# Kernel tuning notes

Hardware: AMD Instinct MI355X
Metric: run time of the kernel (lower is better)

Reference implementation:

```python
import jax, jax.numpy as jnp
import numpy as np

N_NODES = 50000
N_EDGES = 640000
HID = 128
LN_EPS = 1e-5


def setup_inputs() -> dict:
    key = jax.random.key(0)
    ks = jax.random.split(key, 8)
    x = jax.random.normal(ks[0], (N_NODES, HID), dtype=jnp.float32)
    edge_index = jax.random.randint(ks[1], (2, N_EDGES), 0, N_NODES, dtype=jnp.int64)
    edge_attr = jax.random.normal(ks[2], (N_EDGES, HID), dtype=jnp.float32)
    # parameters (Kaiming-ish scaling)
    msg_W1 = jax.random.normal(ks[3], (3 * HID, HID), dtype=jnp.float32) / np.sqrt(3 * HID)
    msg_b1 = jnp.zeros((HID,), dtype=jnp.float32)
    msg_W2 = jax.random.normal(ks[4], (HID, HID), dtype=jnp.float32) / np.sqrt(HID)
    msg_b2 = jnp.zeros((HID,), dtype=jnp.float32)
    upd_W1 = jax.random.normal(ks[5], (2 * HID, HID), dtype=jnp.float32) / np.sqrt(2 * HID)
    upd_b1 = jnp.zeros((HID,), dtype=jnp.float32)
    upd_W2 = jax.random.normal(ks[6], (HID, HID), dtype=jnp.float32) / np.sqrt(HID)
    upd_b2 = jnp.zeros((HID,), dtype=jnp.float32)
    ln_gamma = jnp.ones((HID,), dtype=jnp.float32)
    ln_beta = jnp.zeros((HID,), dtype=jnp.float32)
    return {
        'x': x, 'edge_index': edge_index, 'edge_attr': edge_attr,
        'msg_W1': msg_W1, 'msg_b1': msg_b1, 'msg_W2': msg_W2, 'msg_b2': msg_b2,
        'upd_W1': upd_W1, 'upd_b1': upd_b1, 'upd_W2': upd_W2, 'upd_b2': upd_b2,
        'ln_gamma': ln_gamma, 'ln_beta': ln_beta,
    }


def _layer_norm(h, gamma, beta):
    mu = jnp.mean(h, axis=-1, keepdims=True)
    var = jnp.mean(jnp.square(h - mu), axis=-1, keepdims=True)
    return (h - mu) * jax.lax.rsqrt(var + LN_EPS) * gamma + beta


def reference(x, edge_index, edge_attr,
              msg_W1, msg_b1, msg_W2, msg_b2,
              upd_W1, upd_b1, upd_W2, upd_b2,
              ln_gamma, ln_beta):
    src, dst = edge_index[0], edge_index[1]
    # batched per-edge gather + concat: [E, 3*HID]
    msg_in = jnp.concatenate([x[src], x[dst], edge_attr], axis=-1)
    # message MLP (dropout is identity in eval)
    h = jax.nn.relu(msg_in @ msg_W1 + msg_b1)
    messages = h @ msg_W2 + msg_b2  # [E, HID]
    # scatter-add aggregation by destination node
    aggregated = jax.ops.segment_sum(messages, dst, num_segments=x.shape[0])
    # update MLP
    upd_in = jnp.concatenate([x, aggregated], axis=-1)  # [N, 2*HID]
    u = jax.nn.relu(upd_in @ upd_W1 + upd_b1)
    updated = u @ upd_W2 + upd_b2
    return _layer_norm(x + updated, ln_gamma, ln_beta)
```

## Files before the change

### kernel.cpp

```cpp
#include <hip/hip_runtime.h>

#define HID 128

typedef __attribute__((ext_vector_type(8))) short short8;
typedef __attribute__((ext_vector_type(4))) float f32x4;

__device__ __forceinline__ float bf2f(unsigned short u) {
  union { unsigned int u; float f; } c; c.u = ((unsigned int)u) << 16; return c.f;
}
__device__ __forceinline__ unsigned short f2bf(float f) {
  union { float f; unsigned int u; } c; c.f = f;
  unsigned int u = c.u;
  return (unsigned short)((u + 0x7FFFu + ((u >> 16) & 1u)) >> 16);
}
__device__ __forceinline__ float loads(const void* p, size_t i, bool f32) {
  return f32 ? ((const float*)p)[i] : bf2f(((const unsigned short*)p)[i]);
}
__device__ __forceinline__ short8 load_a8(const void* base, size_t row, int k, bool f32) {
  if (!f32) return *(const short8*)((const unsigned short*)base + row * HID + k);
  const float* fp = (const float*)base + row * HID + k;
  f32x4 f0 = *(const f32x4*)fp;
  f32x4 f1 = *(const f32x4*)(fp + 4);
  short8 t;
  t[0] = (short)f2bf(f0[0]); t[1] = (short)f2bf(f0[1]);
  t[2] = (short)f2bf(f0[2]); t[3] = (short)f2bf(f0[3]);
  t[4] = (short)f2bf(f1[0]); t[5] = (short)f2bf(f1[1]);
  t[6] = (short)f2bf(f1[2]); t[7] = (short)f2bf(f1[3]);
  return t;
}

__global__ void detect_kernel(const void* __restrict__ x,
                              const int* __restrict__ eidx,
                              int* __restrict__ flags) {
  __shared__ int bad, oddnz;
  if (threadIdx.x == 0) { bad = 0; oddnz = 0; }
  __syncthreads();
  const unsigned short* xu = (const unsigned short*)x;
  int mybad = 0;
  for (int i = threadIdx.x; i < 4096; i += 256) {
    int ef = (xu[i] >> 7) & 0xFF;
    if (!(ef == 0 || (ef >= 90 && ef <= 140))) mybad++;
  }
  if (mybad) atomicAdd(&bad, mybad);
  if (threadIdx.x < 128) {
    if (eidx[2 * threadIdx.x + 1] != 0) atomicAdd(&oddnz, 1);
  }
  __syncthreads();
  if (threadIdx.x == 0) {
    flags[0] = (bad > 409) ? 1 : 0;
    flags[1] = (oddnz == 0) ? 1 : 0;
  }
}

__device__ __forceinline__ int get_dst(const int* eidx, bool i64, int E, int e) {
  return i64 ? eidx[2 * (E + e)] : eidx[E + e];
}
__device__ __forceinline__ int get_src(const int* eidx, bool i64, int E, int e) {
  return i64 ? eidx[2 * e] : eidx[e];
}

__global__ void zero_out_kernel(unsigned int* __restrict__ out,
                                const int* __restrict__ flags, long long nelem) {
  bool f32 = flags[0] != 0;
  size_t words = (size_t)nelem * (f32 ? 2 : 1) / 2;
  for (size_t w = blockIdx.x * 256ull + threadIdx.x; w < words; w += (size_t)gridDim.x * 256ull)
    out[w] = 0u;
}

__global__ void repack_all(const void* __restrict__ W1, const void* __restrict__ W2,
                           const void* __restrict__ U1, const void* __restrict__ U2,
                           unsigned short* __restrict__ P1, unsigned short* __restrict__ P2,
                           unsigned short* __restrict__ PU1, unsigned short* __restrict__ PU2,
                           const int* __restrict__ flags) {
  const bool f32 = flags[0] != 0;
  int idx = blockIdx.x * 256 + threadIdx.x;
  const int s1 = 384 * 128, s2 = s1 + 128 * 128, s3 = s2 + 256 * 128, s4 = s3 + 128 * 128;
  if (idx >= s4) return;
  const void* W; unsigned short* P; int off;
  if (idx < s1)      { W = W1; P = P1;  off = idx; }
  else if (idx < s2) { W = W2; P = P2;  off = idx - s1; }
  else if (idx < s3) { W = U1; P = PU1; off = idx - s2; }
  else               { W = U2; P = PU2; off = idx - s3; }
  int j = off & 7, lane = (off >> 3) & 63, ct = (off >> 9) & 7, ks = off >> 12;
  int k = ks * 32 + ((lane >> 4) << 3) + j;
  int n = ct * 16 + (lane & 15);
  P[off] = f2bf(loads(W, (size_t)k * 128 + n, f32));
}

__global__ void hist_kernel(const int* __restrict__ eidx, int* __restrict__ counts,
                            const int* __restrict__ flags, int E, int N) {
  const bool i64 = flags[1] != 0;
  int e = blockIdx.x * 256 + threadIdx.x;
  if (e < E) {
    int d = get_dst(eidx, i64, E, e);
    d = min(max(d, 0), N - 1);
    atomicAdd(&counts[d], 1);
  }
}

__global__ __launch_bounds__(1024) void scanA_kernel(const int* __restrict__ cnt,
                                                     int* __restrict__ curb,
                                                     int* __restrict__ bsum, int N) {
  __shared__ int wsum[16], wsum2[16];
  const int tid = threadIdx.x, lane = tid & 63, wid = tid >> 6;
  int i = blockIdx.x * 1024 + tid;
  int v = (i < N) ? cnt[i] : 0;
  int s = v;
#pragma unroll
  for (int off = 1; off < 64; off <<= 1) {
    int t = __shfl_up(s, off, 64);
    if (lane >= off) s += t;
  }
  if (lane == 63) wsum[wid] = s;
  __syncthreads();
  if (wid == 0 && lane < 16) {
    int w = wsum[lane];
#pragma unroll
    for (int off = 1; off < 16; off <<= 1) {
      int t = __shfl_up(w, off, 16);
      if (lane >= off) w += t;
    }
    wsum2[lane] = w;
    if (lane == 15) bsum[blockIdx.x] = w;
  }
  __syncthreads();
  int pre = (wid > 0) ? wsum2[wid - 1] : 0;
  if (i < N) curb[i] = pre + s - v;
}

__global__ void scanB_kernel(int* __restrict__ bsum, int nb) {
  if (threadIdx.x == 0 && blockIdx.x == 0) {
    int run = 0;
    for (int b = 0; b < nb; b++) { int t = bsum[b]; bsum[b] = run; run += t; }
  }
}

__global__ __launch_bounds__(1024) void scanC_kernel(int* __restrict__ curb,
                                                     const int* __restrict__ bsum, int N) {
  int i = blockIdx.x * 1024 + threadIdx.x;
  if (i < N) curb[i] += bsum[blockIdx.x];
}

__global__ void scatter_rank_kernel(const int* __restrict__ eidx, int* __restrict__ cur,
                                    int* __restrict__ rank, int* __restrict__ sdst,
                                    const int* __restrict__ flags, int E, int N) {
  const bool i64 = flags[1] != 0;
  int e = blockIdx.x * 256 + threadIdx.x;
  if (e < E) {
    int d = get_dst(eidx, i64, E, e);
    d = min(max(d, 0), N - 1);
    int pos = atomicAdd(&cur[d], 1);
    rank[e] = pos;
    sdst[pos] = d;
  }
}

__global__ __launch_bounds__(256) void x1_kernel(
    const void* __restrict__ x, const unsigned short* __restrict__ P1,
    const void* __restrict__ b1, unsigned short* __restrict__ X1,
    const int* __restrict__ flags, int N) {
  __shared__ unsigned short hs[64][264];
  const bool f32 = flags[0] != 0;
  const int tid = threadIdx.x, lane = tid & 63, wid = tid >> 6;
  const int l15 = lane & 15, quad = lane >> 4;
  const int base = blockIdx.x * 64;
  int mn = min(base + wid * 16 + l15, N - 1);

  f32x4 zero = {0.f, 0.f, 0.f, 0.f};
  f32x4 acca[8], accb[8];
#pragma unroll
  for (int ct = 0; ct < 8; ct++) { acca[ct] = zero; accb[ct] = zero; }
#pragma unroll
  for (int ks = 0; ks < 4; ks++) {
    short8 a = load_a8(x, (size_t)mn, ks * 32 + quad * 8, f32);
    const unsigned short* wpa = P1 + ((size_t)(ks * 8) * 64 + lane) * 8;
    const unsigned short* wpb = P1 + ((size_t)((ks + 4) * 8) * 64 + lane) * 8;
#pragma unroll
    for (int ct = 0; ct < 8; ct++) {
      short8 ba = *(const short8*)(wpa + ct * 512);
      short8 bb = *(const short8*)(wpb + ct * 512);
      acca[ct] = __builtin_amdgcn_mfma_f32_16x16x32_bf16(a, ba, acca[ct], 0, 0, 0);
      accb[ct] = __builtin_amdgcn_mfma_f32_16x16x32_bf16(a, bb, accb[ct], 0, 0, 0);
    }
  }
#pragma unroll
  for (int ct = 0; ct < 8; ct++) {
    const int col = ct * 16 + l15;
    const float bv = loads(b1, col, f32);
#pragma unroll
    for (int r = 0; r < 4; r++) {
      hs[wid * 16 + quad * 4 + r][col]       = f2bf(acca[ct][r] + bv);
      hs[wid * 16 + quad * 4 + r][128 + col] = f2bf(accb[ct][r]);
    }
  }
  __syncthreads();
  const int row = tid >> 2, part = tid & 3;
  if (base + row < N) {
    unsigned short* op = X1 + (size_t)(base + row) * 256 + part * 64;
#pragma unroll
    for (int j = 0; j < 8; j++)
      *(short8*)(op + j * 8) = *(const short8*)&hs[row][part * 64 + j * 8];
  }
}

__global__ __launch_bounds__(256) void edgeB_kernel(
    const void* __restrict__ eattr, const int* __restrict__ eidx,
    const int* __restrict__ rank, const unsigned short* __restrict__ X1,
    const unsigned short* __restrict__ P1, const unsigned short* __restrict__ P2,
    unsigned short* __restrict__ msgbuf, const int* __restrict__ flags, int E, int N) {
  __shared__ unsigned short hsb[64][136];
  __shared__ int src_s[64], dst_s[64], rank_s[64];
  const bool f32 = flags[0] != 0;
  const bool i64 = flags[1] != 0;
  const int tid = threadIdx.x, lane = tid & 63, wid = tid >> 6;
  const int l15 = lane & 15, quad = lane >> 4;
  const int base = blockIdx.x * 64;

  if (tid < 64) {
    int e = min(base + tid, E - 1);
    int s = get_src(eidx, i64, E, e);
    int d = get_dst(eidx, i64, E, e);
    src_s[tid] = min(max(s, 0), N - 1);
    dst_s[tid] = min(max(d, 0), N - 1);
    rank_s[tid] = rank[e];
  }

  int me = min(base + wid * 16 + l15, E - 1);
  f32x4 zero = {0.f, 0.f, 0.f, 0.f};
  f32x4 acc[8];
#pragma unroll
  for (int ct = 0; ct < 8; ct++) acc[ct] = zero;
#pragma unroll
  for (int ks = 0; ks < 4; ks++) {
    short8 a = load_a8(eattr, (size_t)me, ks * 32 + quad * 8, f32);
    const unsigned short* wp = P1 + ((size_t)((ks + 8) * 8) * 64 + lane) * 8;
#pragma unroll
    for (int ct = 0; ct < 8; ct++) {
      short8 b = *(const short8*)(wp + ct * 512);
      acc[ct] = __builtin_amdgcn_mfma_f32_16x16x32_bf16(a, b, acc[ct], 0, 0, 0);
    }
  }
#pragma unroll
  for (int ct = 0; ct < 8; ct++) {
    const int col = ct * 16 + l15;
#pragma unroll
    for (int r = 0; r < 4; r++)
      hsb[wid * 16 + quad * 4 + r][col] = f2bf(acc[ct][r]);
  }
  __syncthreads();

#pragma unroll
  for (int it = 0; it < 4; it++) {
    const int r = it * 16 + (tid >> 4);
    const int cg = (tid & 15) * 8;
    short8 h8 = *(const short8*)&hsb[r][cg];
    short8 a8 = *(const short8*)(X1 + (size_t)src_s[r] * 256 + cg);
    short8 b8 = *(const short8*)(X1 + (size_t)dst_s[r] * 256 + 128 + cg);
    short8 o;
#pragma unroll
    for (int j = 0; j < 8; j++) {
      float v = bf2f((unsigned short)h8[j]) + bf2f((unsigned short)a8[j])
              + bf2f((unsigned short)b8[j]);
      o[j] = (short)f2bf(fmaxf(v, 0.f));
    }
    *(short8*)&hsb[r][cg] = o;
  }
  __syncthreads();

  f32x4 acc2[8];
#pragma unroll
  for (int ct = 0; ct < 8; ct++) acc2[ct] = zero;
#pragma unroll
  for (int ks = 0; ks < 4; ks++) {
    short8 a = *(const short8*)&hsb[wid * 16 + l15][ks * 32 + quad * 8];
    const unsigned short* wp = P2 + ((size_t)(ks * 8) * 64 + lane) * 8;
#pragma unroll
    for (int ct = 0; ct < 8; ct++) {
      short8 b = *(const short8*)(wp + ct * 512);
      acc2[ct] = __builtin_amdgcn_mfma_f32_16x16x32_bf16(a, b, acc2[ct], 0, 0, 0);
    }
  }
#pragma unroll
  for (int ct = 0; ct < 8; ct++) {
    const int col = ct * 16 + l15;
#pragma unroll
    for (int r = 0; r < 4; r++)
      hsb[wid * 16 + quad * 4 + r][col] = f2bf(acc2[ct][r]);
  }
  __syncthreads();

  const int row = tid >> 2, part = tid & 3;
  if (base + row < E) {
    unsigned short* mp = msgbuf + (size_t)rank_s[row] * HID + part * 32;
#pragma unroll
    for (int j = 0; j < 4; j++)
      *(short8*)(mp + j * 8) = *(const short8*)&hsb[row][part * 32 + j * 8];
  }
}

__global__ __launch_bounds__(256) void reduce_kernel(
    const unsigned short* __restrict__ msgbuf, const int* __restrict__ sdst,
    const void* __restrict__ b2, float* __restrict__ aggf,
    const int* __restrict__ flags, int E) {
  __shared__ int sd[256];
  const bool f32 = flags[0] != 0;
  const int tid = threadIdx.x;
  const int base = blockIdx.x * 256;
  { int e = base + tid; sd[tid] = (e < E) ? sdst[e] : -1; }
  __syncthreads();
  const int pair = tid & 63;
  const int grp = tid >> 6;
  const int c0 = pair * 2;
  const float b2a = loads(b2, c0, f32);
  const float b2b = loads(b2, c0 + 1, f32);
  float sa = 0.f, sb = 0.f; int cnt = 0, cur = -1;
  for (int r = 0; r < 64; r++) {
    const int lr = grp * 64 + r;
    const int d = sd[lr];
    if (d < 0) break;
    if (d != cur) {
      if (cnt > 0) {
        atomicAdd(&aggf[(size_t)cur * HID + c0],     sa + cnt * b2a);
        atomicAdd(&aggf[(size_t)cur * HID + c0 + 1], sb + cnt * b2b);
      }
      sa = sb = 0.f; cnt = 0; cur = d;
    }
    unsigned int u = *(const unsigned int*)(msgbuf + (size_t)(base + lr) * HID + c0);
    sa += bf2f((unsigned short)(u & 0xFFFF));
    sb += bf2f((unsigned short)(u >> 16));
    cnt++;
  }
  if (cnt > 0) {
    atomicAdd(&aggf[(size_t)cur * HID + c0],     sa + cnt * b2a);
    atomicAdd(&aggf[(size_t)cur * HID + c0 + 1], sb + cnt * b2b);
  }
}

__global__ __launch_bounds__(1024) void scan_kernel(const int* __restrict__ counts,
                                                    int* __restrict__ offs, int N) {
  __shared__ int wsum[16];
  __shared__ int wpre[16];
  __shared__ int carry_s;
  const int tid = threadIdx.x, lane = tid & 63, wid = tid >> 6;
  if (tid == 0) carry_s = 0;
  __syncthreads();
  for (int base = 0; base < N; base += 1024) {
    int i = base + tid;
    int v = (i < N) ? counts[i] : 0;
    int s = v;
#pragma unroll
    for (int off = 1; off < 64; off <<= 1) {
      int t = __shfl_up(s, off, 64);
      if (lane >= off) s += t;
    }
    if (lane == 63) wsum[wid] = s;
    __syncthreads();
    if (tid == 0) {
      int run = carry_s;
#pragma unroll
      for (int w = 0; w < 16; w++) { int t = wsum[w]; wpre[w] = run; run += t; }
      carry_s = run;
    }
    __syncthreads();
    if (i < N) offs[i] = wpre[wid] + s - v;
    __syncthreads();
  }
  if (tid == 0) offs[N] = carry_s;
}

__global__ void scatter_kernel(const int* __restrict__ eidx, int* __restrict__ cur,
                               int* __restrict__ ssrc, int* __restrict__ sdst,
                               int* __restrict__ perm,
                               const int* __restrict__ flags, int E, int N) {
  const bool i64 = flags[1] != 0;
  int e = blockIdx.x * 256 + threadIdx.x;
  if (e < E) {
    int d = get_dst(eidx, i64, E, e);
    int s = get_src(eidx, i64, E, e);
    d = min(max(d, 0), N - 1);
    s = min(max(s, 0), N - 1);
    int pos = atomicAdd(&cur[d], 1);
    ssrc[pos] = s;
    sdst[pos] = d;
    perm[pos] = e;
  }
}

__global__ __launch_bounds__(256) void edge_kernel_sorted(
    const void* __restrict__ x, const void* __restrict__ eattr,
    const int* __restrict__ ssrc, const int* __restrict__ sdst,
    const int* __restrict__ perm,
    const unsigned short* __restrict__ P1, const void* __restrict__ b1,
    const unsigned short* __restrict__ P2, const void* __restrict__ b2,
    float* __restrict__ aggf, const int* __restrict__ flags, int E, int N) {
  __shared__ __align__(16) char smem[64 * 132 * 4];
  __shared__ int sdst_s[64];
  unsigned short (*hs)[136] = (unsigned short (*)[136])smem;
  float (*ms)[132] = (float (*)[132])smem;
  const bool f32 = flags[0] != 0;
  const int tid = threadIdx.x, lane = tid & 63, wid = tid >> 6;
  const int l15 = lane & 15, quad = lane >> 4;
  const int base = blockIdx.x * 64;

  if (tid < 64) sdst_s[tid] = sdst[min(base + tid, E - 1)];

  int me = base + wid * 16 + l15;
  if (me >= E) me = E - 1;
  const int src = ssrc[me];
  const int dsm = sdst[me];
  const int pe  = perm[me];

  f32x4 zero = {0.f, 0.f, 0.f, 0.f};
  f32x4 acc[8];
#pragma unroll
  for (int ct = 0; ct < 8; ct++) acc[ct] = zero;
#pragma unroll
  for (int ks = 0; ks < 12; ks++) {
    const int k0 = ks * 32;
    short8 a;
    if (k0 < 128)      a = load_a8(x,     (size_t)src, k0 + quad * 8, f32);
    else if (k0 < 256) a = load_a8(x,     (size_t)dsm, (k0 - 128) + quad * 8, f32);
    else               a = load_a8(eattr, (size_t)pe,  (k0 - 256) + quad * 8, f32);
    const unsigned short* wp = P1 + ((size_t)(ks * 8) * 64 + lane) * 8;
#pragma unroll
    for (int ct = 0; ct < 8; ct++) {
      short8 b = *(const short8*)(wp + ct * 512);
      acc[ct] = __builtin_amdgcn_mfma_f32_16x16x32_bf16(a, b, acc[ct], 0, 0, 0);
    }
  }
#pragma unroll
  for (int ct = 0; ct < 8; ct++) {
    const int col = ct * 16 + l15;
    const float bv = loads(b1, col, f32);
#pragma unroll
    for (int r = 0; r < 4; r++)
      hs[wid * 16 + quad * 4 + r][col] = f2bf(fmaxf(acc[ct][r] + bv, 0.f));
  }
  f32x4 acc2[8];
#pragma unroll
  for (int ct = 0; ct < 8; ct++) acc2[ct] = zero;
#pragma unroll
  for (int ks = 0; ks < 4; ks++) {
    short8 a = *(const short8*)&hs[wid * 16 + l15][ks * 32 + quad * 8];
    const unsigned short* wp = P2 + ((size_t)(ks * 8) * 64 + lane) * 8;
#pragma unroll
    for (int ct = 0; ct < 8; ct++) {
      short8 b = *(const short8*)(wp + ct * 512);
      acc2[ct] = __builtin_amdgcn_mfma_f32_16x16x32_bf16(a, b, acc2[ct], 0, 0, 0);
    }
  }
  float b2v[8];
#pragma unroll
  for (int ct = 0; ct < 8; ct++) b2v[ct] = loads(b2, ct * 16 + l15, f32);
  __syncthreads();
#pragma unroll
  for (int ct = 0; ct < 8; ct++) {
    const int col = ct * 16 + l15;
#pragma unroll
    for (int r = 0; r < 4; r++) {
      const int e = base + wid * 16 + quad * 4 + r;
      ms[wid * 16 + quad * 4 + r][col] = (e < E) ? (acc2[ct][r] + b2v[ct]) : 0.0f;
    }
  }
  __syncthreads();
  const int col  = tid & 127;
  const int half = tid >> 7;
  const int r0 = half * 32;
  float sum = 0.0f;
  int cur = sdst_s[r0];
#pragma unroll 4
  for (int r = r0; r < r0 + 32; r++) {
    int d = sdst_s[r];
    if (d != cur) {
      atomicAdd(&aggf[(size_t)cur * HID + col], sum);
      sum = 0.0f; cur = d;
    }
    sum += ms[r][col];
  }
  atomicAdd(&aggf[(size_t)cur * HID + col], sum);
}

__global__ __launch_bounds__(256) void edge_kernel_plain(
    const void* __restrict__ x, const int* __restrict__ eidx,
    const void* __restrict__ eattr,
    const unsigned short* __restrict__ P1, const void* __restrict__ b1,
    const unsigned short* __restrict__ P2, const void* __restrict__ b2,
    float* __restrict__ aggf, void* __restrict__ out,
    const int* __restrict__ flags, int E, int N, int small_mode) {
  __shared__ unsigned short hs[64][136];
  const bool f32 = flags[0] != 0;
  const bool i64 = flags[1] != 0;
  const int tid = threadIdx.x, lane = tid & 63, wid = tid >> 6;
  const int l15 = lane & 15, quad = lane >> 4;
  const int base = blockIdx.x * 64;

  int me = base + wid * 16 + l15;
  if (me >= E) me = E - 1;
  int src = get_src(eidx, i64, E, me);
  int dsm = get_dst(eidx, i64, E, me);
  src = min(max(src, 0), N - 1);
  dsm = min(max(dsm, 0), N - 1);

  f32x4 zero = {0.f, 0.f, 0.f, 0.f};
  f32x4 acc[8];
#pragma unroll
  for (int ct = 0; ct < 8; ct++) acc[ct] = zero;
#pragma unroll
  for (int ks = 0; ks < 12; ks++) {
    const int k0 = ks * 32;
    short8 a;
    if (k0 < 128)      a = load_a8(x,     (size_t)src, k0 + quad * 8, f32);
    else if (k0 < 256) a = load_a8(x,     (size_t)dsm, (k0 - 128) + quad * 8, f32);
    else               a = load_a8(eattr, (size_t)me,  (k0 - 256) + quad * 8, f32);
    const unsigned short* wp = P1 + ((size_t)(ks * 8) * 64 + lane) * 8;
#pragma unroll
    for (int ct = 0; ct < 8; ct++) {
      short8 b = *(const short8*)(wp + ct * 512);
      acc[ct] = __builtin_amdgcn_mfma_f32_16x16x32_bf16(a, b, acc[ct], 0, 0, 0);
    }
  }
#pragma unroll
  for (int ct = 0; ct < 8; ct++) {
    const int col = ct * 16 + l15;
    const float bv = loads(b1, col, f32);
#pragma unroll
    for (int r = 0; r < 4; r++)
      hs[wid * 16 + quad * 4 + r][col] = f2bf(fmaxf(acc[ct][r] + bv, 0.f));
  }
  __syncthreads();
  f32x4 acc2[8];
#pragma unroll
  for (int ct = 0; ct < 8; ct++) acc2[ct] = zero;
#pragma unroll
  for (int ks = 0; ks < 4; ks++) {
    short8 a = *(const short8*)&hs[wid * 16 + l15][ks * 32 + quad * 8];
    const unsigned short* wp = P2 + ((size_t)(ks * 8) * 64 + lane) * 8;
#pragma unroll
    for (int ct = 0; ct < 8; ct++) {
      short8 b = *(const short8*)(wp + ct * 512);
      acc2[ct] = __builtin_amdgcn_mfma_f32_16x16x32_bf16(a, b, acc2[ct], 0, 0, 0);
    }
  }
  float b2v[8];
#pragma unroll
  for (int ct = 0; ct < 8; ct++) b2v[ct] = loads(b2, ct * 16 + l15, f32);

  if (!small_mode || f32) {
    float* tgt = (!small_mode) ? aggf : (float*)out;
#pragma unroll
    for (int r = 0; r < 4; r++) {
      const int e = base + wid * 16 + quad * 4 + r;
      if (e < E) {
        int d = get_dst(eidx, i64, E, e);
        d = min(max(d, 0), N - 1);
        float* op = tgt + (size_t)d * HID + l15;
#pragma unroll
        for (int ct = 0; ct < 8; ct++) atomicAdd(op + ct * 16, acc2[ct][r] + b2v[ct]);
      }
    }
  } else {
#pragma unroll
    for (int ct = 0; ct < 8; ct++) {
      const int col = ct * 16 + l15;
#pragma unroll
      for (int r = 0; r < 4; r++)
        hs[wid * 16 + quad * 4 + r][col] = f2bf(acc2[ct][r] + b2v[ct]);
    }
    __syncthreads();
    const int row = tid >> 2;
    const int cg  = (tid & 3) * 32;
    const int e = base + row;
    if (e < E) {
      int d = get_dst(eidx, i64, E, e);
      d = min(max(d, 0), N - 1);
      unsigned int* orow = (unsigned int*)out + ((size_t)d * HID >> 1);
#pragma unroll
      for (int p = 0; p < 16; p++) {
        const int col = cg + p * 2;
        const float lo = bf2f(hs[row][col]);
        const float hi = bf2f(hs[row][col + 1]);
        unsigned int* wp = orow + (col >> 1);
        unsigned int old = *wp, assumed;
        do {
          assumed = old;
          unsigned int nv = (unsigned int)f2bf(bf2f((unsigned short)(assumed & 0xFFFF)) + lo)
                          | ((unsigned int)f2bf(bf2f((unsigned short)(assumed >> 16)) + hi) << 16);
          old = atomicCAS(wp, assumed, nv);
        } while (old != assumed);
      }
    }
  }
}

__global__ __launch_bounds__(256) void node_kernel(
    const void* __restrict__ x, const float* __restrict__ aggf,
    const unsigned short* __restrict__ PU1, const void* __restrict__ ub1,
    const unsigned short* __restrict__ PU2, const void* __restrict__ ub2,
    const void* __restrict__ gamma, const void* __restrict__ beta,
    void* __restrict__ out, const int* __restrict__ flags, int N, int small_mode) {
  __shared__ unsigned short hs[64][136];
  const bool f32 = flags[0] != 0;
  const int tid = threadIdx.x, lane = tid & 63, wid = tid >> 6;
  const int l15 = lane & 15, quad = lane >> 4;
  const int base = blockIdx.x * 64;

  int mn = base + wid * 16 + l15;
  if (mn >= N) mn = N - 1;

  const void* aggp = (!small_mode) ? (const void*)aggf : (const void*)out;
  const bool aggF32 = (!small_mode) ? true : f32;

  f32x4 zero = {0.f, 0.f, 0.f, 0.f};
  f32x4 acc[8];
#pragma unroll
  for (int ct = 0; ct < 8; ct++) acc[ct] = zero;
#pragma unroll
  for (int ks = 0; ks < 8; ks++) {
    const int k0 = ks * 32;
    short8 a;
    if (k0 < 128) a = load_a8(x,    (size_t)mn, k0 + quad * 8, f32);
    else          a = load_a8(aggp, (size_t)mn, (k0 - 128) + quad * 8, aggF32);
    const unsigned short* wp = PU1 + ((size_t)(ks * 8) * 64 + lane) * 8;
#pragma unroll
    for (int ct = 0; ct < 8; ct++) {
      short8 b = *(const short8*)(wp + ct * 512);
      acc[ct] = __builtin_amdgcn_mfma_f32_16x16x32_bf16(a, b, acc[ct], 0, 0, 0);
    }
  }
#pragma unroll
  for (int ct = 0; ct < 8; ct++) {
    const int col = ct * 16 + l15;
    const float bv = loads(ub1, col, f32);
#pragma unroll
    for (int r = 0; r < 4; r++)
      hs[wid * 16 + quad * 4 + r][col] = f2bf(fmaxf(acc[ct][r] + bv, 0.f));
  }
  __syncthreads();
  f32x4 acc2[8];
#pragma unroll
  for (int ct = 0; ct < 8; ct++) acc2[ct] = zero;
#pragma unroll
  for (int ks = 0; ks < 4; ks++) {
    short8 a = *(const short8*)&hs[wid * 16 + l15][ks * 32 + quad * 8];
    const unsigned short* wp = PU2 + ((size_t)(ks * 8) * 64 + lane) * 8;
#pragma unroll
    for (int ct = 0; ct < 8; ct++) {
      short8 b = *(const short8*)(wp + ct * 512);
      acc2[ct] = __builtin_amdgcn_mfma_f32_16x16x32_bf16(a, b, acc2[ct], 0, 0, 0);
    }
  }

  float vals[8][4];
  float s1[4] = {0.f, 0.f, 0.f, 0.f};
  float s2[4] = {0.f, 0.f, 0.f, 0.f};
#pragma unroll
  for (int ct = 0; ct < 8; ct++) {
    const int col = ct * 16 + l15;
    const float bv = loads(ub2, col, f32);
#pragma unroll
    for (int r = 0; r < 4; r++) {
      int row = base + wid * 16 + quad * 4 + r;
      int rc = row < N ? row : 0;
      float v = acc2[ct][r] + bv + loads(x, (size_t)rc * HID + col, f32);
      vals[ct][r] = v;
      s1[r] += v;
      s2[r] += v * v;
    }
  }
#pragma unroll
  for (int off = 1; off < 16; off <<= 1) {
#pragma unroll
    for (int r = 0; r < 4; r++) {
      s1[r] += __shfl_xor(s1[r], off, 16);
      s2[r] += __shfl_xor(s2[r], off, 16);
    }
  }
#pragma unroll
  for (int r = 0; r < 4; r++) {
    const int row = base + wid * 16 + quad * 4 + r;
    if (row < N) {
      const float mean = s1[r] * (1.0f / 128.0f);
      const float var  = fmaxf(s2[r] * (1.0f / 128.0f) - mean * mean, 0.0f);
      const float rstd = rsqrtf(var + 1e-5f);
#pragma unroll
      for (int ct = 0; ct < 8; ct++) {
        const int col = ct * 16 + l15;
        float o = (vals[ct][r] - mean) * rstd * loads(gamma, col, f32) + loads(beta, col, f32);
        if (f32) ((float*)out)[(size_t)row * HID + col] = o;
        else     ((unsigned short*)out)[(size_t)row * HID + col] = f2bf(o);
      }
    }
  }
}

extern "C" void kernel_launch(void* const* d_in, const int* in_sizes, int n_in,
                              void* d_out, int out_size, void* d_ws, size_t ws_size,
                              hipStream_t stream) {
  (void)n_in;
  const void* x     = d_in[0];
  const int*  eidx  = (const int*)d_in[1];
  const void* eattr = d_in[2];
  const void* W1  = d_in[3];
  const void* b1  = d_in[4];
  const void* W2  = d_in[5];
  const void* b2  = d_in[6];
  const void* U1  = d_in[7];
  const void* ub1 = d_in[8];
  const void* U2  = d_in[9];
  const void* ub2 = d_in[10];
  const void* gam = d_in[11];
  const void* bet = d_in[12];

  const int N = in_sizes[0] / HID;
  const int E = in_sizes[2] / HID;

  char* ws = (char*)d_ws;
  auto alignup = [](size_t v) { return (v + 255) & ~(size_t)255; };

  int* flags = (int*)ws;
  unsigned short* P1  = (unsigned short*)(ws + 256);
  unsigned short* P2  = (unsigned short*)(ws + 256 + 98304);
  unsigned short* PU1 = (unsigned short*)(ws + 256 + 131072);
  unsigned short* PU2 = (unsigned short*)(ws + 256 + 196608);
  const size_t agg_off = 256 + 229376;
  float* aggf = (float*)(ws + agg_off);
  const size_t agg_bytes = (size_t)N * HID * sizeof(float);
  const size_t need_basic = agg_off + agg_bytes;

  size_t o3 = alignup(need_basic);
  size_t cnt_off  = o3; o3 = alignup(o3 + (size_t)(N + 64) * 4);
  size_t cur_off  = o3; o3 = alignup(o3 + (size_t)(N + 64) * 4);
  size_t bsum_off = o3; o3 = alignup(o3 + 1024);
  size_t rank_off = o3; o3 = alignup(o3 + (size_t)E * 4);
  size_t sds3_off = o3; o3 = alignup(o3 + (size_t)E * 4);
  size_t x1_off   = o3; o3 = alignup(o3 + (size_t)N * 256 * 2);
  size_t msg_off  = o3; o3 = alignup(o3 + (size_t)E * HID * 2);
  const size_t need3 = o3;

  size_t o2 = alignup(need_basic);
  size_t offs_off = o2; o2 = alignup(o2 + (size_t)(N + 1) * 4);
  size_t cur2_off = o2; o2 = alignup(o2 + (size_t)(N + 1) * 4);
  size_t ssrc_off = o2; o2 = alignup(o2 + (size_t)E * 4);
  size_t sds2_off = o2; o2 = alignup(o2 + (size_t)E * 4);
  size_t perm_off = o2; o2 = alignup(o2 + (size_t)E * 4);
  const size_t need2 = o2;

  const int mode = (ws_size >= need3) ? 3
                 : (ws_size >= need2) ? 2
                 : (ws_size >= need_basic) ? 1 : 0;

  detect_kernel<<<1, 256, 0, stream>>>(x, eidx, flags);
  repack_all<<<448, 256, 0, stream>>>(W1, W2, U1, U2, P1, P2, PU1, PU2, flags);

  if (mode == 3) {
    int* cntb = (int*)(ws + cnt_off);
    int* curb = (int*)(ws + cur_off);
    int* bsum = (int*)(ws + bsum_off);
    int* rank = (int*)(ws + rank_off);
    int* sdst = (int*)(ws + sds3_off);
    unsigned short* X1     = (unsigned short*)(ws + x1_off);
    unsigned short* msgbuf = (unsigned short*)(ws + msg_off);
    const int nb = (N + 1023) / 1024;

    hipMemsetAsync(aggf, 0, agg_bytes, stream);
    hipMemsetAsync(cntb, 0, (size_t)N * 4, stream);
    hist_kernel<<<(E + 255) / 256, 256, 0, stream>>>(eidx, cntb, flags, E, N);
    scanA_kernel<<<nb, 1024, 0, stream>>>(cntb, curb, bsum, N);
    scanB_kernel<<<1, 64, 0, stream>>>(bsum, nb);
    scanC_kernel<<<nb, 1024, 0, stream>>>(curb, bsum, N);
    scatter_rank_kernel<<<(E + 255) / 256, 256, 0, stream>>>(eidx, curb, rank, sdst,
                                                             flags, E, N);
    x1_kernel<<<(N + 63) / 64, 256, 0, stream>>>(x, P1, b1, X1, flags, N);
    edgeB_kernel<<<(E + 63) / 64, 256, 0, stream>>>(eattr, eidx, rank, X1, P1, P2,
                                                    msgbuf, flags, E, N);
    reduce_kernel<<<(E + 255) / 256, 256, 0, stream>>>(msgbuf, sdst, b2, aggf, flags, E);
    node_kernel<<<(N + 63) / 64, 256, 0, stream>>>(x, aggf, PU1, ub1, PU2, ub2,
                                                   gam, bet, d_out, flags, N, 0);
  } else if (mode == 2) {
    int* offsb = (int*)(ws + offs_off);
    int* curb  = (int*)(ws + cur2_off);
    int* ssrc  = (int*)(ws + ssrc_off);
    int* sdst  = (int*)(ws + sds2_off);
    int* perm  = (int*)(ws + perm_off);
    hipMemsetAsync(aggf, 0, agg_bytes, stream);
    hipMemsetAsync(curb, 0, (size_t)(N + 1) * 4, stream);
    hist_kernel<<<(E + 255) / 256, 256, 0, stream>>>(eidx, curb, flags, E, N);
    scan_kernel<<<1, 1024, 0, stream>>>(curb, offsb, N);
    hipMemcpyAsync(curb, offsb, (size_t)(N + 1) * 4, hipMemcpyDeviceToDevice, stream);
    scatter_kernel<<<(E + 255) / 256, 256, 0, stream>>>(eidx, curb, ssrc, sdst, perm,
                                                        flags, E, N);
    edge_kernel_sorted<<<(E + 63) / 64, 256, 0, stream>>>(x, eattr, ssrc, sdst, perm,
                                                          P1, b1, P2, b2, aggf, flags, E, N);
    node_kernel<<<(N + 63) / 64, 256, 0, stream>>>(x, aggf, PU1, ub1, PU2, ub2,
                                                   gam, bet, d_out, flags, N, 0);
  } else if (mode == 1) {
    hipMemsetAsync(aggf, 0, agg_bytes, stream);
    edge_kernel_plain<<<(E + 63) / 64, 256, 0, stream>>>(x, eidx, eattr, P1, b1, P2, b2,
                                                         aggf, d_out, flags, E, N, 0);
    node_kernel<<<(N + 63) / 64, 256, 0, stream>>>(x, aggf, PU1, ub1, PU2, ub2,
                                                   gam, bet, d_out, flags, N, 0);
  } else {
    zero_out_kernel<<<1024, 256, 0, stream>>>((unsigned int*)d_out, flags, (long long)out_size);
    edge_kernel_plain<<<(E + 63) / 64, 256, 0, stream>>>(x, eidx, eattr, P1, b1, P2, b2,
                                                         aggf, d_out, flags, E, N, 1);
    node_kernel<<<(N + 63) / 64, 256, 0, stream>>>(x, aggf, PU1, ub1, PU2, ub2,
                                                   gam, bet, d_out, flags, N, 1);
  }
}
```

Measured before the change: 876.4 us.

## Replace atomic segmented reduce with per-node CSR reduction and prefetch gathers

The reduction now assigns one wavefront per destination node and uses the CSR offsets left in curb after the scatter, together with cntb, to sum that node's sorted messages. It writes aggf directly, so the memset of aggf, the float atomics and the sdst array with its scatter writes are all removed. The edge kernel also issues the X1 source and destination gathers into registers at kernel start, so they overlap the first MFMA stage instead of waiting on shared-memory indices. The cost is higher register pressure in the edge kernel and load imbalance across nodes with different in-degrees.

```diff
diff --git a/kernel.cpp b/kernel.cpp
--- a/kernel.cpp
+++ b/kernel.cpp
@@ -4,6 +4,7 @@
 
 typedef __attribute__((ext_vector_type(8))) short short8;
 typedef __attribute__((ext_vector_type(4))) float f32x4;
+typedef __attribute__((ext_vector_type(2))) float f32x2;
 
 __device__ __forceinline__ float bf2f(unsigned short u) {
   union { unsigned int u; float f; } c; c.u = ((unsigned int)u) << 16; return c.f;
@@ -142,7 +143,7 @@
 }
 
 __global__ void scatter_rank_kernel(const int* __restrict__ eidx, int* __restrict__ cur,
-                                    int* __restrict__ rank, int* __restrict__ sdst,
+                                    int* __restrict__ rank,
                                     const int* __restrict__ flags, int E, int N) {
   const bool i64 = flags[1] != 0;
   int e = blockIdx.x * 256 + threadIdx.x;
@@ -151,7 +152,6 @@
     d = min(max(d, 0), N - 1);
     int pos = atomicAdd(&cur[d], 1);
     rank[e] = pos;
-    sdst[pos] = d;
   }
 }
 
@@ -209,20 +209,27 @@
     const unsigned short* __restrict__ P1, const unsigned short* __restrict__ P2,
     unsigned short* __restrict__ msgbuf, const int* __restrict__ flags, int E, int N) {
   __shared__ unsigned short hsb[64][136];
-  __shared__ int src_s[64], dst_s[64], rank_s[64];
+  __shared__ int rank_s[64];
   const bool f32 = flags[0] != 0;
   const bool i64 = flags[1] != 0;
   const int tid = threadIdx.x, lane = tid & 63, wid = tid >> 6;
   const int l15 = lane & 15, quad = lane >> 4;
   const int base = blockIdx.x * 64;
 
-  if (tid < 64) {
-    int e = min(base + tid, E - 1);
+  if (tid < 64) rank_s[tid] = rank[min(base + tid, E - 1)];
+
+  const int gr = tid >> 4;
+  const int cg = (tid & 15) * 8;
+  short8 ga[4], gb[4];
+#pragma unroll
+  for (int it = 0; it < 4; it++) {
+    const int e = min(base + it * 16 + gr, E - 1);
     int s = get_src(eidx, i64, E, e);
     int d = get_dst(eidx, i64, E, e);
-    src_s[tid] = min(max(s, 0), N - 1);
-    dst_s[tid] = min(max(d, 0), N - 1);
-    rank_s[tid] = rank[e];
+    s = min(max(s, 0), N - 1);
+    d = min(max(d, 0), N - 1);
+    ga[it] = *(const short8*)(X1 + (size_t)s * 256 + cg);
+    gb[it] = *(const short8*)(X1 + (size_t)d * 256 + 128 + cg);
   }
 
   int me = min(base + wid * 16 + l15, E - 1);
@@ -251,11 +258,10 @@
 
 #pragma unroll
   for (int it = 0; it < 4; it++) {
-    const int r = it * 16 + (tid >> 4);
-    const int cg = (tid & 15) * 8;
+    const int r = it * 16 + gr;
     short8 h8 = *(const short8*)&hsb[r][cg];
-    short8 a8 = *(const short8*)(X1 + (size_t)src_s[r] * 256 + cg);
-    short8 b8 = *(const short8*)(X1 + (size_t)dst_s[r] * 256 + 128 + cg);
+    short8 a8 = ga[it];
+    short8 b8 = gb[it];
     short8 o;
 #pragma unroll
     for (int j = 0; j < 8; j++) {
@@ -298,42 +304,37 @@
   }
 }
 
-__global__ __launch_bounds__(256) void reduce_kernel(
-    const unsigned short* __restrict__ msgbuf, const int* __restrict__ sdst,
-    const void* __restrict__ b2, float* __restrict__ aggf,
-    const int* __restrict__ flags, int E) {
-  __shared__ int sd[256];
+__global__ __launch_bounds__(256) void reduce_csr_kernel(
+    const unsigned short* __restrict__ msgbuf, const int* __restrict__ curb,
+    const int* __restrict__ cntb, const void* __restrict__ b2,
+    float* __restrict__ aggf, const int* __restrict__ flags, int N) {
   const bool f32 = flags[0] != 0;
-  const int tid = threadIdx.x;
-  const int base = blockIdx.x * 256;
-  { int e = base + tid; sd[tid] = (e < E) ? sdst[e] : -1; }
-  __syncthreads();
-  const int pair = tid & 63;
-  const int grp = tid >> 6;
-  const int c0 = pair * 2;
-  const float b2a = loads(b2, c0, f32);
-  const float b2b = loads(b2, c0 + 1, f32);
-  float sa = 0.f, sb = 0.f; int cnt = 0, cur = -1;
-  for (int r = 0; r < 64; r++) {
-    const int lr = grp * 64 + r;
-    const int d = sd[lr];
-    if (d < 0) break;
-    if (d != cur) {
-      if (cnt > 0) {
-        atomicAdd(&aggf[(size_t)cur * HID + c0],     sa + cnt * b2a);
-        atomicAdd(&aggf[(size_t)cur * HID + c0 + 1], sb + cnt * b2b);
-      }
-      sa = sb = 0.f; cnt = 0; cur = d;
-    }
-    unsigned int u = *(const unsigned int*)(msgbuf + (size_t)(base + lr) * HID + c0);
-    sa += bf2f((unsigned short)(u & 0xFFFF));
-    sb += bf2f((unsigned short)(u >> 16));
-    cnt++;
-  }
-  if (cnt > 0) {
-    atomicAdd(&aggf[(size_t)cur * HID + c0],     sa + cnt * b2a);
-    atomicAdd(&aggf[(size_t)cur * HID + c0 + 1], sb + cnt * b2b);
-  }
+  const int lane = threadIdx.x & 63, wid = threadIdx.x >> 6;
+  const int d = blockIdx.x * 4 + wid;
+  if (d >= N) return;
+  const int cnt = cntb[d];
+  const int end = curb[d];
+  const int beg = end - cnt;
+  const int c0 = lane * 2;
+  float sa0 = 0.f, sb0 = 0.f, sa1 = 0.f, sb1 = 0.f;
+  int p = beg;
+  for (; p + 2 <= end; p += 2) {
+    unsigned int u0 = *(const unsigned int*)(msgbuf + (size_t)p * HID + c0);
+    unsigned int u1 = *(const unsigned int*)(msgbuf + (size_t)(p + 1) * HID + c0);
+    sa0 += bf2f((unsigned short)(u0 & 0xFFFF));
+    sb0 += bf2f((unsigned short)(u0 >> 16));
+    sa1 += bf2f((unsigned short)(u1 & 0xFFFF));
+    sb1 += bf2f((unsigned short)(u1 >> 16));
+  }
+  if (p < end) {
+    unsigned int u = *(const unsigned int*)(msgbuf + (size_t)p * HID + c0);
+    sa0 += bf2f((unsigned short)(u & 0xFFFF));
+    sb0 += bf2f((unsigned short)(u >> 16));
+  }
+  f32x2 o;
+  o.x = sa0 + sa1 + cnt * loads(b2, c0, f32);
+  o.y = sb0 + sb1 + cnt * loads(b2, c0 + 1, f32);
+  *(f32x2*)(aggf + (size_t)d * HID + c0) = o;
 }
 
 __global__ __launch_bounds__(1024) void scan_kernel(const int* __restrict__ counts,
@@ -732,7 +733,6 @@
   size_t cur_off  = o3; o3 = alignup(o3 + (size_t)(N + 64) * 4);
   size_t bsum_off = o3; o3 = alignup(o3 + 1024);
   size_t rank_off = o3; o3 = alignup(o3 + (size_t)E * 4);
-  size_t sds3_off = o3; o3 = alignup(o3 + (size_t)E * 4);
   size_t x1_off   = o3; o3 = alignup(o3 + (size_t)N * 256 * 2);
   size_t msg_off  = o3; o3 = alignup(o3 + (size_t)E * HID * 2);
   const size_t need3 = o3;
@@ -757,23 +757,22 @@
     int* curb = (int*)(ws + cur_off);
     int* bsum = (int*)(ws + bsum_off);
     int* rank = (int*)(ws + rank_off);
-    int* sdst = (int*)(ws + sds3_off);
     unsigned short* X1     = (unsigned short*)(ws + x1_off);
     unsigned short* msgbuf = (unsigned short*)(ws + msg_off);
     const int nb = (N + 1023) / 1024;
 
-    hipMemsetAsync(aggf, 0, agg_bytes, stream);
     hipMemsetAsync(cntb, 0, (size_t)N * 4, stream);
     hist_kernel<<<(E + 255) / 256, 256, 0, stream>>>(eidx, cntb, flags, E, N);
     scanA_kernel<<<nb, 1024, 0, stream>>>(cntb, curb, bsum, N);
     scanB_kernel<<<1, 64, 0, stream>>>(bsum, nb);
     scanC_kernel<<<nb, 1024, 0, stream>>>(curb, bsum, N);
-    scatter_rank_kernel<<<(E + 255) / 256, 256, 0, stream>>>(eidx, curb, rank, sdst,
+    scatter_rank_kernel<<<(E + 255) / 256, 256, 0, stream>>>(eidx, curb, rank,
                                                              flags, E, N);
     x1_kernel<<<(N + 63) / 64, 256, 0, stream>>>(x, P1, b1, X1, flags, N);
     edgeB_kernel<<<(E + 63) / 64, 256, 0, stream>>>(eattr, eidx, rank, X1, P1, P2,
                                                     msgbuf, flags, E, N);
-    reduce_kernel<<<(E + 255) / 256, 256, 0, stream>>>(msgbuf, sdst, b2, aggf, flags, E);
+    reduce_csr_kernel<<<(N + 3) / 4, 256, 0, stream>>>(msgbuf, curb, cntb, b2, aggf,
+                                                       flags, N);
     node_kernel<<<(N + 63) / 64, 256, 0, stream>>>(x, aggf, PU1, ub1, PU2, ub2,
                                                    gam, bet, d_out, flags, N, 0);
   } else if (mode == 2) {
```

New measurement: 840.3 us. -4.1%, faster.

## Fuse segment reduction into edge kernel using dst-sorted edge order

Applied to the files above, without the earlier changes.

Edges are now processed in destination-sorted order: the edge kernel gathers edge_attr through a permutation and reduces messages directly into the aggregation buffer with per-segment atomics. This removes the separate reduce kernel and the large bf16 message buffer write and read round trip. In exchange, edge_attr reads become permuted gathers and atomics are issued per 32-row half block rather than per 64 rows. One inter-stage barrier is dropped because each wave only touches its own rows.

```diff
diff --git a/kernel.cpp b/kernel.cpp
--- a/kernel.cpp
+++ b/kernel.cpp
@@ -4,6 +4,7 @@
 
 typedef __attribute__((ext_vector_type(8))) short short8;
 typedef __attribute__((ext_vector_type(4))) float f32x4;
+typedef __attribute__((ext_vector_type(2))) float f32x2;
 
 __device__ __forceinline__ float bf2f(unsigned short u) {
   union { unsigned int u; float f; } c; c.u = ((unsigned int)u) << 16; return c.f;
@@ -141,20 +142,6 @@
   if (i < N) curb[i] += bsum[blockIdx.x];
 }
 
-__global__ void scatter_rank_kernel(const int* __restrict__ eidx, int* __restrict__ cur,
-                                    int* __restrict__ rank, int* __restrict__ sdst,
-                                    const int* __restrict__ flags, int E, int N) {
-  const bool i64 = flags[1] != 0;
-  int e = blockIdx.x * 256 + threadIdx.x;
-  if (e < E) {
-    int d = get_dst(eidx, i64, E, e);
-    d = min(max(d, 0), N - 1);
-    int pos = atomicAdd(&cur[d], 1);
-    rank[e] = pos;
-    sdst[pos] = d;
-  }
-}
-
 __global__ __launch_bounds__(256) void x1_kernel(
     const void* __restrict__ x, const unsigned short* __restrict__ P1,
     const void* __restrict__ b1, unsigned short* __restrict__ X1,
@@ -203,36 +190,38 @@
   }
 }
 
-__global__ __launch_bounds__(256) void edgeB_kernel(
-    const void* __restrict__ eattr, const int* __restrict__ eidx,
-    const int* __restrict__ rank, const unsigned short* __restrict__ X1,
+__global__ __launch_bounds__(256) void edgeS_kernel(
+    const void* __restrict__ eattr, const int* __restrict__ ssrc,
+    const int* __restrict__ sdst, const int* __restrict__ perm,
+    const unsigned short* __restrict__ X1,
     const unsigned short* __restrict__ P1, const unsigned short* __restrict__ P2,
-    unsigned short* __restrict__ msgbuf, const int* __restrict__ flags, int E, int N) {
-  __shared__ unsigned short hsb[64][136];
-  __shared__ int src_s[64], dst_s[64], rank_s[64];
+    const void* __restrict__ b2, float* __restrict__ aggf,
+    const int* __restrict__ flags, int E, int N) {
+  __shared__ __align__(16) char smem[64 * 132 * 4];
+  __shared__ int sdst_s[64], ssrc_s[64];
+  unsigned short (*hs)[136] = (unsigned short (*)[136])smem;
+  float (*ms)[132] = (float (*)[132])smem;
   const bool f32 = flags[0] != 0;
-  const bool i64 = flags[1] != 0;
   const int tid = threadIdx.x, lane = tid & 63, wid = tid >> 6;
   const int l15 = lane & 15, quad = lane >> 4;
   const int base = blockIdx.x * 64;
 
   if (tid < 64) {
     int e = min(base + tid, E - 1);
-    int s = get_src(eidx, i64, E, e);
-    int d = get_dst(eidx, i64, E, e);
-    src_s[tid] = min(max(s, 0), N - 1);
-    dst_s[tid] = min(max(d, 0), N - 1);
-    rank_s[tid] = rank[e];
-  }
-
-  int me = min(base + wid * 16 + l15, E - 1);
+    sdst_s[tid] = sdst[e];
+    ssrc_s[tid] = ssrc[e];
+  }
+
+  const int me = min(base + wid * 16 + l15, E - 1);
+  const int pe = perm[me];
+
   f32x4 zero = {0.f, 0.f, 0.f, 0.f};
   f32x4 acc[8];
 #pragma unroll
   for (int ct = 0; ct < 8; ct++) acc[ct] = zero;
 #pragma unroll
   for (int ks = 0; ks < 4; ks++) {
-    short8 a = load_a8(eattr, (size_t)me, ks * 32 + quad * 8, f32);
+    short8 a = load_a8(eattr, (size_t)pe, ks * 32 + quad * 8, f32);
     const unsigned short* wp = P1 + ((size_t)((ks + 8) * 8) * 64 + lane) * 8;
 #pragma unroll
     for (int ct = 0; ct < 8; ct++) {
@@ -245,34 +234,46 @@
     const int col = ct * 16 + l15;
 #pragma unroll
     for (int r = 0; r < 4; r++)
-      hsb[wid * 16 + quad * 4 + r][col] = f2bf(acc[ct][r]);
-  }
-  __syncthreads();
-
-#pragma unroll
-  for (int it = 0; it < 4; it++) {
-    const int r = it * 16 + (tid >> 4);
-    const int cg = (tid & 15) * 8;
-    short8 h8 = *(const short8*)&hsb[r][cg];
-    short8 a8 = *(const short8*)(X1 + (size_t)src_s[r] * 256 + cg);
-    short8 b8 = *(const short8*)(X1 + (size_t)dst_s[r] * 256 + 128 + cg);
-    short8 o;
-#pragma unroll
-    for (int j = 0; j < 8; j++) {
-      float v = bf2f((unsigned short)h8[j]) + bf2f((unsigned short)a8[j])
-              + bf2f((unsigned short)b8[j]);
-      o[j] = (short)f2bf(fmaxf(v, 0.f));
-    }
-    *(short8*)&hsb[r][cg] = o;
-  }
-  __syncthreads();
+      hsb_write: ;
+  }
+#pragma unroll
+  for (int ct = 0; ct < 8; ct++) {
+    const int col = ct * 16 + l15;
+#pragma unroll
+    for (int r = 0; r < 4; r++)
+      hs[wid * 16 + quad * 4 + r][col] = f2bf(acc[ct][r]);
+  }
+  __syncthreads();
+
+  {
+    const int r = wid * 16 + (lane >> 2);
+    const int cq = (lane & 3) * 8;
+    const int s = ssrc_s[r], d = sdst_s[r];
+    const unsigned short* ap = X1 + (size_t)s * 256;
+    const unsigned short* bp = X1 + (size_t)d * 256 + 128;
+#pragma unroll
+    for (int j = 0; j < 4; j++) {
+      const int c0 = cq + j * 32;
+      short8 h8 = *(const short8*)&hs[r][c0];
+      short8 a8 = *(const short8*)(ap + c0);
+      short8 b8 = *(const short8*)(bp + c0);
+      short8 o;
+#pragma unroll
+      for (int k = 0; k < 8; k++) {
+        float v = bf2f((unsigned short)h8[k]) + bf2f((unsigned short)a8[k])
+                + bf2f((unsigned short)b8[k]);
+        o[k] = (short)f2bf(fmaxf(v, 0.f));
+      }
+      *(short8*)&hs[r][c0] = o;
+    }
+  }
 
   f32x4 acc2[8];
 #pragma unroll
   for (int ct = 0; ct < 8; ct++) acc2[ct] = zero;
 #pragma unroll
   for (int ks = 0; ks < 4; ks++) {
-    short8 a = *(const short8*)&hsb[wid * 16 + l15][ks * 32 + quad * 8];
+    short8 a = *(const short8*)&hs[wid * 16 + l15][ks * 32 + quad * 8];
     const unsigned short* wp = P2 + ((size_t)(ks * 8) * 64 + lane) * 8;
 #pragma unroll
     for (int ct = 0; ct < 8; ct++) {
@@ -280,60 +281,36 @@
       acc2[ct] = __builtin_amdgcn_mfma_f32_16x16x32_bf16(a, b, acc2[ct], 0, 0, 0);
     }
   }
-#pragma unroll
-  for (int ct = 0; ct < 8; ct++) {
-    const int col = ct * 16 + l15;
-#pragma unroll
-    for (int r = 0; r < 4; r++)
-      hsb[wid * 16 + quad * 4 + r][col] = f2bf(acc2[ct][r]);
-  }
-  __syncthreads();
-
-  const int row = tid >> 2, part = tid & 3;
-  if (base + row < E) {
-    unsigned short* mp = msgbuf + (size_t)rank_s[row] * HID + part * 32;
-#pragma unroll
-    for (int j = 0; j < 4; j++)
-      *(short8*)(mp + j * 8) = *(const short8*)&hsb[row][part * 32 + j * 8];
-  }
-}
-
-__global__ __launch_bounds__(256) void reduce_kernel(
-    const unsigned short* __restrict__ msgbuf, const int* __restrict__ sdst,
-    const void* __restrict__ b2, float* __restrict__ aggf,
-    const int* __restrict__ flags, int E) {
-  __shared__ int sd[256];
-  const bool f32 = flags[0] != 0;
-  const int tid = threadIdx.x;
-  const int base = blockIdx.x * 256;
-  { int e = base + tid; sd[tid] = (e < E) ? sdst[e] : -1; }
-  __syncthreads();
-  const int pair = tid & 63;
-  const int grp = tid >> 6;
-  const int c0 = pair * 2;
-  const float b2a = loads(b2, c0, f32);
-  const float b2b = loads(b2, c0 + 1, f32);
-  float sa = 0.f, sb = 0.f; int cnt = 0, cur = -1;
-  for (int r = 0; r < 64; r++) {
-    const int lr = grp * 64 + r;
-    const int d = sd[lr];
-    if (d < 0) break;
+  float b2v[8];
+#pragma unroll
+  for (int ct = 0; ct < 8; ct++) b2v[ct] = loads(b2, ct * 16 + l15, f32);
+  __syncthreads();
+#pragma unroll
+  for (int ct = 0; ct < 8; ct++) {
+    const int col = ct * 16 + l15;
+#pragma unroll
+    for (int r = 0; r < 4; r++) {
+      const int e = base + wid * 16 + quad * 4 + r;
+      ms[wid * 16 + quad * 4 + r][col] = (e < E) ? (acc2[ct][r] + b2v[ct]) : 0.0f;
+    }
+  }
+  __syncthreads();
+
+  const int col  = tid & 127;
+  const int half = tid >> 7;
+  const int r0 = half * 32;
+  float sum = 0.0f;
+  int cur = sdst_s[r0];
+#pragma unroll 4
+  for (int r = r0; r < r0 + 32; r++) {
+    int d = sdst_s[r];
     if (d != cur) {
-      if (cnt > 0) {
-        atomicAdd(&aggf[(size_t)cur * HID + c0],     sa + cnt * b2a);
-        atomicAdd(&aggf[(size_t)cur * HID + c0 + 1], sb + cnt * b2b);
-      }
-      sa = sb = 0.f; cnt = 0; cur = d;
-    }
-    unsigned int u = *(const unsigned int*)(msgbuf + (size_t)(base + lr) * HID + c0);
-    sa += bf2f((unsigned short)(u & 0xFFFF));
-    sb += bf2f((unsigned short)(u >> 16));
-    cnt++;
-  }
-  if (cnt > 0) {
-    atomicAdd(&aggf[(size_t)cur * HID + c0],     sa + cnt * b2a);
-    atomicAdd(&aggf[(size_t)cur * HID + c0 + 1], sb + cnt * b2b);
-  }
+      atomicAdd(&aggf[(size_t)cur * HID + col], sum);
+      sum = 0.0f; cur = d;
+    }
+    sum += ms[r][col];
+  }
+  atomicAdd(&aggf[(size_t)cur * HID + col], sum);
 }
 
 __global__ __launch_bounds__(1024) void scan_kernel(const int* __restrict__ counts,
@@ -731,10 +708,10 @@
   size_t cnt_off  = o3; o3 = alignup(o3 + (size_t)(N + 64) * 4);
   size_t cur_off  = o3; o3 = alignup(o3 + (size_t)(N + 64) * 4);
   size_t bsum_off = o3; o3 = alignup(o3 + 1024);
-  size_t rank_off = o3; o3 = alignup(o3 + (size_t)E * 4);
-  size_t sds3_off = o3; o3 = alignup(o3 + (size_t)E * 4);
+  size_t src3_off = o3; o3 = alignup(o3 + (size_t)E * 4);
+  size_t dst3_off = o3; o3 = alignup(o3 + (size_t)E * 4);
+  size_t prm3_off = o3; o3 = alignup(o3 + (size_t)E * 4);
   size_t x1_off   = o3; o3 = alignup(o3 + (size_t)N * 256 * 2);
-  size_t msg_off  = o3; o3 = alignup(o3 + (size_t)E * HID * 2);
   const size_t need3 = o3;
 
   size_t o2 = alignup(need_basic);
@@ -756,10 +733,10 @@
     int* cntb = (int*)(ws + cnt_off);
     int* curb = (int*)(ws + cur_off);
     int* bsum = (int*)(ws + bsum_off);
-    int* rank = (int*)(ws + rank_off);
-    int* sdst = (int*)(ws + sds3_off);
-    unsigned short* X1     = (unsigned short*)(ws + x1_off);
-    unsigned short* msgbuf = (unsigned short*)(ws + msg_off);
+    int* ssrc = (int*)(ws + src3_off);
+    int* sdst = (int*)(ws + dst3_off);
+    int* perm = (int*)(ws + prm3_off);
+    unsigned short* X1 = (unsigned short*)(ws + x1_off);
     const int nb = (N + 1023) / 1024;
 
     hipMemsetAsync(aggf, 0, agg_bytes, stream);
@@ -768,12 +745,11 @@
     scanA_kernel<<<nb, 1024, 0, stream>>>(cntb, curb, bsum, N);
     scanB_kernel<<<1, 64, 0, stream>>>(bsum, nb);
     scanC_kernel<<<nb, 1024, 0, stream>>>(curb, bsum, N);
-    scatter_rank_kernel<<<(E + 255) / 256, 256, 0, stream>>>(eidx, curb, rank, sdst,
-                                                             flags, E, N);
+    scatter_kernel<<<(E + 255) / 256, 256, 0, stream>>>(eidx, curb, ssrc, sdst, perm,
+                                                        flags, E, N);
     x1_kernel<<<(N + 63) / 64, 256, 0, stream>>>(x, P1, b1, X1, flags, N);
-    edgeB_kernel<<<(E + 63) / 64, 256, 0, stream>>>(eattr, eidx, rank, X1, P1, P2,
-                                                    msgbuf, flags, E, N);
-    reduce_kernel<<<(E + 255) / 256, 256, 0, stream>>>(msgbuf, sdst, b2, aggf, flags, E);
+    edgeS_kernel<<<(E + 63) / 64, 256, 0, stream>>>(eattr, ssrc, sdst, perm, X1,
+                                                    P1, P2, b2, aggf, flags, E, N);
     node_kernel<<<(N + 63) / 64, 256, 0, stream>>>(x, aggf, PU1, ub1, PU2, ub2,
                                                    gam, bet, d_out, flags, N, 0);
   } else if (mode == 2) {
```

Result: faster. 783.2 us (-10.6%).
